# Optimization experiments

Hardware: AMD Instinct MI355X
Metric: run time of the kernel (lower is better)

Reference implementation:

```python
import jax, jax.numpy as jnp
import numpy as np

N, E, IN_DIM, HID, HEADS = 50000, 400000, 128, 64, 4
NEG_SLOPE, LN_EPS = 0.2, 1e-5


def setup_inputs() -> dict:
    key = jax.random.key(0)
    ks = jax.random.split(key, 12)
    x = jax.random.normal(ks[0], (N, IN_DIM), dtype=jnp.float32)
    edge_index = jax.random.randint(ks[1], (2, E), 0, N, dtype=jnp.int64)
    s = 1.0 / np.sqrt(HID)
    return {
        "x": x,
        "edge_index": edge_index,
        "W_gcn": jax.random.normal(ks[2], (IN_DIM, HID), dtype=jnp.float32) / np.sqrt(IN_DIM),
        "b_gcn": jnp.zeros((HID,), dtype=jnp.float32),
        "W_gat": jax.random.normal(ks[3], (HID, HEADS * HID), dtype=jnp.float32) * s,
        "att_src": jax.random.normal(ks[4], (HEADS, HID), dtype=jnp.float32) * s,
        "att_dst": jax.random.normal(ks[5], (HEADS, HID), dtype=jnp.float32) * s,
        "b_gat": jnp.zeros((HID,), dtype=jnp.float32),
        "W_patch": jax.random.normal(ks[6], (HID, HID), dtype=jnp.float32) * s,
        "b_patch": jnp.zeros((HID,), dtype=jnp.float32),
        "gamma": jnp.ones((HID,), dtype=jnp.float32),
        "beta": jnp.zeros((HID,), dtype=jnp.float32),
    }


def _forward(x, edge_index, W_gcn, b_gcn, W_gat, att_src, att_dst, b_gat,
             W_patch, b_patch, gamma, beta):
    n = x.shape[0]
    loop = jnp.arange(n, dtype=edge_index.dtype)
    src = jnp.concatenate([edge_index[0], loop])  # self-loops appended (PyG default)
    dst = jnp.concatenate([edge_index[1], loop])

    # ---- GCNConv: symmetric degree normalization + scatter-add ----
    deg = jax.ops.segment_sum(jnp.ones_like(dst, dtype=jnp.float32), dst, num_segments=n)
    dinv = jnp.where(deg > 0, jax.lax.rsqrt(deg), 0.0)
    norm = dinv[src] * dinv[dst]  # [E+N]
    xw = x @ W_gcn  # [N,HID]
    h1 = jax.ops.segment_sum(xw[src] * norm[:, None], dst, num_segments=n) + b_gcn
    h1 = jax.nn.relu(h1)

    # ---- GATConv (heads=4, concat=False -> mean over heads) ----
    z = (h1 @ W_gat).reshape(n, HEADS, HID)  # [N,H,C]
    a_s = jnp.einsum('nhc,hc->nh', z, att_src)  # [N,H]
    a_d = jnp.einsum('nhc,hc->nh', z, att_dst)
    e = jax.nn.leaky_relu(a_s[src] + a_d[dst], negative_slope=NEG_SLOPE)  # [E+N,H]
    # segment-softmax over incoming edges per destination node
    m = jax.ops.segment_max(e, dst, num_segments=n)  # [N,H]
    ex = jnp.exp(e - m[dst])
    denom = jax.ops.segment_sum(ex, dst, num_segments=n)
    alpha = ex / denom[dst]  # [E+N,H]
    agg = jax.ops.segment_sum(z[src] * alpha[:, :, None], dst, num_segments=n)  # [N,H,C]
    h2 = jax.nn.relu(agg.mean(axis=1) + b_gat)

    # ---- residual fusion + LayerNorm (dropout is identity in eval) ----
    h_patch = h1 @ W_patch + b_patch
    h = h1 + h2 + h_patch
    mu = h.mean(axis=-1, keepdims=True)
    var = h.var(axis=-1, keepdims=True)
    return (h - mu) * jax.lax.rsqrt(var + LN_EPS) * gamma + beta


def reference(x, edge_index, W_gcn, b_gcn, W_gat, att_src, att_dst, b_gat,
              W_patch, b_patch, gamma, beta):
    return _forward(x, edge_index, W_gcn, b_gcn, W_gat, att_src, att_dst, b_gat,
                    W_patch, b_patch, gamma, beta)
```

## Files before the change

### kernel.cpp

```cpp
#include <hip/hip_runtime.h>
#include <math.h>

#define IN_DIM 128
#define HID 64
#define HEADS 4
#define NEG_SLOPE 0.2f
#define LN_EPS 1e-5f
#define APAD 328

typedef short bf16x8 __attribute__((ext_vector_type(8)));
typedef float f32x4  __attribute__((ext_vector_type(4)));
typedef unsigned short u16x4 __attribute__((ext_vector_type(4)));
typedef unsigned long long ull;

__device__ inline unsigned short f2bf(float f) {
    unsigned u = __float_as_uint(f);
    u += 0x7fffu + ((u >> 16) & 1u);
    return (unsigned short)(u >> 16);
}
__device__ inline float bf2f(unsigned short s) {
    return __uint_as_float(((unsigned)s) << 16);
}
__device__ inline float leaky(float v) { return v > 0.0f ? v : NEG_SLOPE * v; }

__global__ __launch_bounds__(256) void k_init(const void* ei, int E, int n,
                           int* flag, int* hist, ull* A,
                           const float* __restrict__ Wg, const float* __restrict__ Wp,
                           const float* __restrict__ Wgcn,
                           const float* __restrict__ att_s, const float* __restrict__ att_d,
                           unsigned short* __restrict__ Wt_post,
                           unsigned short* __restrict__ Wt_xw,
                           float* __restrict__ w_s, float* __restrict__ w_d) {
    int t = threadIdx.x;
    int role = blockIdx.x;
    if (role < 14) {
        int p = role * 256 + t;
        if (p < 2560) {
            int c = p & 63, kg = p >> 6;
            bf16x8 v;
#pragma unroll
            for (int j = 0; j < 8; j++) {
                int k = kg * 8 + j;
                float f;
                if (k < 256) f = 0.25f * Wg[(size_t)(k & 63) * 256 + (k >> 6) * 64 + c];
                else         f = Wp[(size_t)(k - 256) * 64 + c];
                v[j] = (short)f2bf(f);
            }
            *(bf16x8*)(&Wt_post[(size_t)p * 8]) = v;
        } else if (p < 2560 + 1024) {
            int q = p - 2560;
            int c = q & 63, kg = q >> 6;
            bf16x8 v;
#pragma unroll
            for (int j = 0; j < 8; j++)
                v[j] = (short)f2bf(Wgcn[(size_t)(kg * 8 + j) * 64 + c]);
            *(bf16x8*)(&Wt_xw[(size_t)q * 8]) = v;
        }
        return;
    }
    if (role == 14) {
        A[t] = 0ULL;
        __shared__ int s_bad;
        if (t == 0) s_bad = 0;
        __syncthreads();
        int lim = E < 4096 ? E : 4096;
        int bad = 0;
        for (int k = t; k < lim; k += 256)
            if (((const ull*)ei)[k] >= (ull)n) bad = 1;
        if (bad) s_bad = 1;
        __syncthreads();
        if (t == 0) *flag = s_bad ? 0 : 1;
        int h = t >> 6, k = t & 63;
        float ss = 0.0f, sd = 0.0f;
        for (int c = 0; c < HID; c++) {
            float w = Wg[(size_t)k * (HEADS * HID) + h * HID + c];
            ss += w * att_s[h * HID + c];
            sd += w * att_d[h * HID + c];
        }
        w_s[h * HID + k] = ss;
        w_d[h * HID + k] = sd;
        return;
    }
    __shared__ int s_bad2;
    if (t == 0) s_bad2 = 0;
    __syncthreads();
    int lim = E < 4096 ? E : 4096;
    int bad = 0;
    for (int k = t; k < lim; k += 256)
        if (((const ull*)ei)[k] >= (ull)n) bad = 1;
    if (bad) s_bad2 = 1;
    __syncthreads();
    int is64 = s_bad2 ? 0 : 1;
    int hb = role - 15;
    int nhb = gridDim.x - 15;
    for (int i = hb * 256 + t; i < E; i += nhb * 256) {
        int d;
        if (is64) d = (int)((const long long*)ei)[E + i];
        else      d = ((const int*)ei)[E + i];
        atomicAdd(&hist[d], 1);
    }
}

__global__ __launch_bounds__(256) void k_scan_lb(const int* __restrict__ hist,
                                                 ull* __restrict__ A,
                                                 int* __restrict__ row_ptr,
                                                 int* __restrict__ cursor,
                                                 float* __restrict__ dinv, int n) {
    __shared__ int s[256];
    __shared__ int sbase;
    int t = threadIdx.x, c = blockIdx.x;
    int w = t >> 6, lane = t & 63;
    int i = c * 256 + t;
    int v = (i < n) ? hist[i] : 0;
    s[t] = v;
    __syncthreads();
    for (int off = 1; off < 256; off <<= 1) {
        int xv = (t >= off) ? s[t - off] : 0;
        __syncthreads();
        s[t] += xv;
        __syncthreads();
    }
    int incl = s[t];
    int S = s[255];
    if (t == 0) {
        if (c == 0) { sbase = 0; atomicExch(&A[0], (2ULL << 32) | (unsigned)S); }
        else          atomicExch(&A[c], (1ULL << 32) | (unsigned)S);
    }
    if (c > 0 && w == 0) {
        long long run = 0;
        int p = c - 1;
        for (;;) {
            int idx = p - lane;
            unsigned st, val;
            if (idx >= 0) {
                ull v2 = atomicAdd(&A[idx], 0ULL);
                st = (unsigned)(v2 >> 32); val = (unsigned)v2;
            } else { st = 2u; val = 0u; }
            ull pm = __ballot(st == 2);
            ull zm = __ballot(st == 0);
            int firstP = pm ? (__ffsll((long long)pm) - 1) : 64;
            int firstZ = zm ? (__ffsll((long long)zm) - 1) : 64;
            if (firstZ < firstP) { __builtin_amdgcn_s_sleep(1); continue; }
            unsigned contrib = (lane <= firstP) ? val : 0u;
#pragma unroll
            for (int o = 1; o <= 32; o <<= 1) contrib += __shfl_xor(contrib, o, 64);
            run += contrib;
            if (firstP < 64) break;
            p -= 64;
        }
        if (lane == 0) {
            sbase = (int)run;
            atomicExch(&A[c], (2ULL << 32) | (unsigned)(run + (unsigned)S));
        }
    }
    __syncthreads();
    if (i < n) {
        int excl = sbase + incl - v;
        row_ptr[i] = excl;
        cursor[i] = excl;
        dinv[i] = rsqrtf((float)(v + 1));
    }
}

__global__ __launch_bounds__(256) void k_scatter_xw(const void* ei, int E,
                                                    const int* __restrict__ flag,
                                                    int* __restrict__ cursor,
                                                    int* __restrict__ col,
                                                    const float* __restrict__ x,
                                                    const unsigned short* __restrict__ Wt_g,
                                                    const float* __restrict__ dinv,
                                                    unsigned short* __restrict__ xws, int n) {
    __shared__ unsigned short Wt[16 * 64 * 8];
    int nsb = (E + 255) >> 8;
    if ((int)blockIdx.x < nsb) {
        int i = blockIdx.x * 256 + threadIdx.x;
        if (i >= E) return;
        int is64 = *flag;
        int s, d;
        if (is64) { s = (int)((const long long*)ei)[i]; d = (int)((const long long*)ei)[E + i]; }
        else      { s = ((const int*)ei)[i];            d = ((const int*)ei)[E + i]; }
        int pos = atomicAdd(&cursor[d], 1);
        col[pos] = s;
    } else {
        int bx = blockIdx.x - nsb;
        int t = threadIdx.x;
        for (int idx = t; idx < 1024; idx += 256)
            *(bf16x8*)(&Wt[idx * 8]) = *(const bf16x8*)(&Wt_g[(size_t)idx * 8]);
        __syncthreads();
        int lane = t & 63;
        int li = lane & 15, quad = lane >> 4;
        int w = t >> 6;
        int r0 = bx * 64 + w * 16;
        int rload = r0 + li; if (rload > n - 1) rload = n - 1;
        f32x4 acc[4];
#pragma unroll
        for (int i = 0; i < 4; i++) acc[i] = (f32x4){0.f, 0.f, 0.f, 0.f};
        const float* xp = x + (size_t)rload * IN_DIM + quad * 8;
#pragma unroll
        for (int ks = 0; ks < 4; ks++) {
            float4 p0 = *(const float4*)(xp + ks * 32);
            float4 p1 = *(const float4*)(xp + ks * 32 + 4);
            bf16x8 a;
            a[0] = (short)f2bf(p0.x); a[1] = (short)f2bf(p0.y);
            a[2] = (short)f2bf(p0.z); a[3] = (short)f2bf(p0.w);
            a[4] = (short)f2bf(p1.x); a[5] = (short)f2bf(p1.y);
            a[6] = (short)f2bf(p1.z); a[7] = (short)f2bf(p1.w);
            int kg = ks * 4 + quad;
#pragma unroll
            for (int tt = 0; tt < 4; tt++) {
                bf16x8 bfr = *(const bf16x8*)(&Wt[((kg * 64) + tt * 16 + li) * 8]);
                acc[tt] = __builtin_amdgcn_mfma_f32_16x16x32_bf16(a, bfr, acc[tt], 0, 0, 0);
            }
        }
#pragma unroll
        for (int reg = 0; reg < 4; reg++) {
            int r = r0 + quad * 4 + reg;
            if (r >= n) continue;
            float dv = dinv[r];
#pragma unroll
            for (int tt = 0; tt < 4; tt++)
                xws[(size_t)r * HID + tt * 16 + li] = f2bf(acc[tt][reg] * dv);
        }
    }
}

__global__ __launch_bounds__(256) void k_gcn(const int* __restrict__ col,
                                             const int* __restrict__ row_ptr,
                                             const int* __restrict__ hist,
                                             const float* __restrict__ dinv,
                                             const unsigned short* __restrict__ xws,
                                             const float* __restrict__ b,
                                             const float* __restrict__ w_s,
                                             const float* __restrict__ w_d,
                                             unsigned short* __restrict__ h1b,
                                             float4* __restrict__ a_s,
                                             float4* __restrict__ a_d, int n) {
    int t = threadIdx.x;
    int w = t >> 6, lane = t & 63, q = lane >> 4, li = lane & 15;
    int d = blockIdx.x * 4 + w;
    if (d >= n) return;
    int start = row_ptr[d], cnt = hist[d];
    float a0, a1, a2, a3;
    {
        u16x4 sv = *(const u16x4*)(xws + (size_t)d * HID + li * 4);
        float z = (q == 0) ? 1.0f : 0.0f;
        a0 = z * bf2f(sv[0]); a1 = z * bf2f(sv[1]);
        a2 = z * bf2f(sv[2]); a3 = z * bf2f(sv[3]);
    }
    for (int base = 0; base < cnt; base += 64) {
        int m = cnt - base; if (m > 64) m = 64;
        int ci = (lane < m) ? col[start + base + lane] : 0;
        for (int kb = 0; kb < m; kb += 8) {
            int k0 = kb + q, k1 = kb + q + 4;
            int s0 = __shfl(ci, k0, 64);
            int s1 = __shfl(ci, k1 & 63, 64);
            u16x4 v0 = *(const u16x4*)(xws + (size_t)s0 * HID + li * 4);
            u16x4 v1 = *(const u16x4*)(xws + (size_t)s1 * HID + li * 4);
            float g0 = (k0 < m) ? 1.0f : 0.0f;
            float g1 = (k1 < m) ? 1.0f : 0.0f;
            a0 += g0 * bf2f(v0[0]) + g1 * bf2f(v1[0]);
            a1 += g0 * bf2f(v0[1]) + g1 * bf2f(v1[1]);
            a2 += g0 * bf2f(v0[2]) + g1 * bf2f(v1[2]);
            a3 += g0 * bf2f(v0[3]) + g1 * bf2f(v1[3]);
        }
    }
    a0 += __shfl_xor(a0, 16, 64); a1 += __shfl_xor(a1, 16, 64);
    a2 += __shfl_xor(a2, 16, 64); a3 += __shfl_xor(a3, 16, 64);
    a0 += __shfl_xor(a0, 32, 64); a1 += __shfl_xor(a1, 32, 64);
    a2 += __shfl_xor(a2, 32, 64); a3 += __shfl_xor(a3, 32, 64);
    float dv = dinv[d];
    float4 bv = *(const float4*)(b + li * 4);
    float h0 = fmaxf(a0 * dv + bv.x, 0.0f);
    float h1 = fmaxf(a1 * dv + bv.y, 0.0f);
    float h2 = fmaxf(a2 * dv + bv.z, 0.0f);
    float h3 = fmaxf(a3 * dv + bv.w, 0.0f);
    if (q == 0) {
        u16x4 o;
        o[0] = f2bf(h0); o[1] = f2bf(h1); o[2] = f2bf(h2); o[3] = f2bf(h3);
        *(u16x4*)(h1b + (size_t)d * HID + li * 4) = o;
    }
    float4 u  = *(const float4*)(w_s + q * 64 + li * 4);
    float vs = h0 * u.x + h1 * u.y + h2 * u.z + h3 * u.w;
    float4 u2 = *(const float4*)(w_d + q * 64 + li * 4);
    float vd = h0 * u2.x + h1 * u2.y + h2 * u2.z + h3 * u2.w;
#pragma unroll
    for (int o = 1; o <= 8; o <<= 1) {
        vs += __shfl_xor(vs, o, 64);
        vd += __shfl_xor(vd, o, 64);
    }
    float vs1 = __shfl(vs, 16, 64), vs2 = __shfl(vs, 32, 64), vs3 = __shfl(vs, 48, 64);
    float vd1 = __shfl(vd, 16, 64), vd2 = __shfl(vd, 32, 64), vd3 = __shfl(vd, 48, 64);
    if (lane == 0) {
        a_s[d] = make_float4(vs, vs1, vs2, vs3);
        a_d[d] = make_float4(vd, vd1, vd2, vd3);
    }
}

__global__ __launch_bounds__(256) void k_attn_post(
        const int* __restrict__ col, const int* __restrict__ row_ptr,
        const int* __restrict__ hist,
        const float4* __restrict__ a_s, const float4* __restrict__ a_d,
        const unsigned short* __restrict__ h1b,
        const unsigned short* __restrict__ Wt_g,
        const float* __restrict__ bp, const float* __restrict__ bg,
        const float* __restrict__ gamma, const float* __restrict__ beta,
        float* __restrict__ out, int n) {
    __shared__ unsigned short Atile[16 * APAD];
    __shared__ float hbuf[16 * 68];
    int t = threadIdx.x;
    int w = t >> 6, lane = t & 63, q = lane >> 4, li = lane & 15;
    int rowbase = blockIdx.x * 16;

    for (int j = 0; j < 4; j++) {
        int r = w * 4 + j;
        int d = rowbase + r;
        if (d >= n) {
            for (int c = lane; c < 320; c += 64) Atile[r * APAD + c] = 0;
            continue;
        }
        int start = row_ptr[d], cnt = hist[d];
        float4 ad = a_d[d];
        float4 asd = a_s[d];
        u16x4 sv = *(const u16x4*)(h1b + (size_t)d * HID + li * 4);
        float e0 = __expf(leaky(asd.x + ad.x));
        float e1 = __expf(leaky(asd.y + ad.y));
        float e2 = __expf(leaky(asd.z + ad.z));
        float e3 = __expf(leaky(asd.w + ad.w));
        float z = (q == 0) ? 1.0f : 0.0f;
        float f0 = bf2f(sv[0]), f1 = bf2f(sv[1]), f2 = bf2f(sv[2]), f3 = bf2f(sv[3]);
        f32x4 A0 = {z * e0 * f0, z * e0 * f1, z * e0 * f2, z * e0 * f3};
        f32x4 A1 = {z * e1 * f0, z * e1 * f1, z * e1 * f2, z * e1 * f3};
        f32x4 A2 = {z * e2 * f0, z * e2 * f1, z * e2 * f2, z * e2 * f3};
        f32x4 A3 = {z * e3 * f0, z * e3 * f1, z * e3 * f2, z * e3 * f3};
        float l0 = z * e0, l1 = z * e1, l2 = z * e2, l3 = z * e3;
        for (int base = 0; base < cnt; base += 64) {
            int m = cnt - base; if (m > 64) m = 64;
            int ci = (lane < m) ? col[start + base + lane] : 0;
            for (int kb = 0; kb < m; kb += 8) {
                int k0 = kb + q, k1 = kb + q + 4;
                int s0 = __shfl(ci, k0, 64);
                int s1 = __shfl(ci, k1 & 63, 64);
                float4 as0 = a_s[s0];
                float4 as1 = a_s[s1];
                u16x4 hv0 = *(const u16x4*)(h1b + (size_t)s0 * HID + li * 4);
                u16x4 hv1 = *(const u16x4*)(h1b + (size_t)s1 * HID + li * 4);
                bool p0 = (k0 < m), p1 = (k1 < m);
                float w00 = p0 ? __expf(leaky(as0.x + ad.x)) : 0.0f;
                float w01 = p0 ? __expf(leaky(as0.y + ad.y)) : 0.0f;
                float w02 = p0 ? __expf(leaky(as0.z + ad.z)) : 0.0f;
                float w03 = p0 ? __expf(leaky(as0.w + ad.w)) : 0.0f;
                float w10 = p1 ? __expf(leaky(as1.x + ad.x)) : 0.0f;
                float w11 = p1 ? __expf(leaky(as1.y + ad.y)) : 0.0f;
                float w12 = p1 ? __expf(leaky(as1.z + ad.z)) : 0.0f;
                float w13 = p1 ? __expf(leaky(as1.w + ad.w)) : 0.0f;
                float g00 = bf2f(hv0[0]), g01 = bf2f(hv0[1]);
                float g02 = bf2f(hv0[2]), g03 = bf2f(hv0[3]);
                float g10 = bf2f(hv1[0]), g11 = bf2f(hv1[1]);
                float g12 = bf2f(hv1[2]), g13 = bf2f(hv1[3]);
                A0[0] += w00 * g00 + w10 * g10; A0[1] += w00 * g01 + w10 * g11;
                A0[2] += w00 * g02 + w10 * g12; A0[3] += w00 * g03 + w10 * g13;
                A1[0] += w01 * g00 + w11 * g10; A1[1] += w01 * g01 + w11 * g11;
                A1[2] += w01 * g02 + w11 * g12; A1[3] += w01 * g03 + w11 * g13;
                A2[0] += w02 * g00 + w12 * g10; A2[1] += w02 * g01 + w12 * g11;
                A2[2] += w02 * g02 + w12 * g12; A2[3] += w02 * g03 + w12 * g13;
                A3[0] += w03 * g00 + w13 * g10; A3[1] += w03 * g01 + w13 * g11;
                A3[2] += w03 * g02 + w13 * g12; A3[3] += w03 * g03 + w13 * g13;
                l0 += w00 + w10; l1 += w01 + w11;
                l2 += w02 + w12; l3 += w03 + w13;
            }
        }
#pragma unroll
        for (int c4 = 0; c4 < 4; c4++) {
            A0[c4] += __shfl_xor(A0[c4], 16, 64);
            A1[c4] += __shfl_xor(A1[c4], 16, 64);
            A2[c4] += __shfl_xor(A2[c4], 16, 64);
            A3[c4] += __shfl_xor(A3[c4], 16, 64);
        }
        l0 += __shfl_xor(l0, 16, 64); l1 += __shfl_xor(l1, 16, 64);
        l2 += __shfl_xor(l2, 16, 64); l3 += __shfl_xor(l3, 16, 64);
#pragma unroll
        for (int c4 = 0; c4 < 4; c4++) {
            A0[c4] += __shfl_xor(A0[c4], 32, 64);
            A1[c4] += __shfl_xor(A1[c4], 32, 64);
            A2[c4] += __shfl_xor(A2[c4], 32, 64);
            A3[c4] += __shfl_xor(A3[c4], 32, 64);
        }
        l0 += __shfl_xor(l0, 32, 64); l1 += __shfl_xor(l1, 32, 64);
        l2 += __shfl_xor(l2, 32, 64); l3 += __shfl_xor(l3, 32, 64);
        f32x4 Aq; float lq;
        if (q == 0)      { Aq = A0; lq = l0; }
        else if (q == 1) { Aq = A1; lq = l1; }
        else if (q == 2) { Aq = A2; lq = l2; }
        else             { Aq = A3; lq = l3; }
        float inv = 1.0f / lq;
        u16x4 o;
        o[0] = f2bf(Aq[0] * inv); o[1] = f2bf(Aq[1] * inv);
        o[2] = f2bf(Aq[2] * inv); o[3] = f2bf(Aq[3] * inv);
        *(u16x4*)(&Atile[r * APAD + q * 64 + li * 4]) = o;
        if (q == 0) *(u16x4*)(&Atile[r * APAD + 256 + li * 4]) = sv;
    }
    __syncthreads();

    f32x4 acc_a = {0.f, 0.f, 0.f, 0.f}, acc_h = {0.f, 0.f, 0.f, 0.f};
#pragma unroll
    for (int ks = 0; ks < 10; ks++) {
        int kg = ks * 4 + q;
        bf16x8 a = *(const bf16x8*)(&Atile[li * APAD + ks * 32 + q * 8]);
        bf16x8 bb = *(const bf16x8*)(&Wt_g[(size_t)(kg * 64 + w * 16 + li) * 8]);
        if (ks < 8) acc_a = __builtin_amdgcn_mfma_f32_16x16x32_bf16(a, bb, acc_a, 0, 0, 0);
        else        acc_h = __builtin_amdgcn_mfma_f32_16x16x32_bf16(a, bb, acc_h, 0, 0, 0);
    }
    int cc = w * 16 + li;
    float bgv = bg[cc], bpv = bp[cc];
#pragma unroll
    for (int reg = 0; reg < 4; reg++) {
        int r = q * 4 + reg;
        float h1c = bf2f(Atile[r * APAD + 256 + cc]);
        float h2v = fmaxf(acc_a[reg] + bgv, 0.0f);
        hbuf[r * 68 + cc] = h1c + h2v + acc_h[reg] + bpv;
    }
    __syncthreads();

    int row = t >> 4, lj = t & 15;
    f32x4 hv4 = *(const f32x4*)(&hbuf[row * 68 + lj * 4]);
    float s1 = (hv4[0] + hv4[1]) + (hv4[2] + hv4[3]);
    float s2 = (hv4[0] * hv4[0] + hv4[1] * hv4[1]) + (hv4[2] * hv4[2] + hv4[3] * hv4[3]);
#pragma unroll
    for (int o = 1; o <= 8; o <<= 1) {
        s1 += __shfl_xor(s1, o, 64);
        s2 += __shfl_xor(s2, o, 64);
    }
    float mu = s1 * (1.0f / 64.0f);
    float var = s2 * (1.0f / 64.0f) - mu * mu;
    float rs = rsqrtf(var + LN_EPS);
    int rg = rowbase + row;
    if (rg < n) {
        float4 g4 = *(const float4*)(gamma + lj * 4);
        float4 b4 = *(const float4*)(beta + lj * 4);
        float4 ov;
        ov.x = (hv4[0] - mu) * rs * g4.x + b4.x;
        ov.y = (hv4[1] - mu) * rs * g4.y + b4.y;
        ov.z = (hv4[2] - mu) * rs * g4.z + b4.z;
        ov.w = (hv4[3] - mu) * rs * g4.w + b4.w;
        *(float4*)(out + (size_t)rg * HID + lj * 4) = ov;
    }
}

extern "C" void kernel_launch(void* const* d_in, const int* in_sizes, int n_in,
                              void* d_out, int out_size, void* d_ws, size_t ws_size,
                              hipStream_t stream) {
    int n = in_sizes[0] / IN_DIM;
    int E = in_sizes[1] / 2;

    const float* x     = (const float*)d_in[0];
    const void*  ei    = d_in[1];
    const float* W_gcn = (const float*)d_in[2];
    const float* b_gcn = (const float*)d_in[3];
    const float* W_gat = (const float*)d_in[4];
    const float* att_s = (const float*)d_in[5];
    const float* att_d = (const float*)d_in[6];
    const float* b_gat = (const float*)d_in[7];
    const float* W_p   = (const float*)d_in[8];
    const float* b_p   = (const float*)d_in[9];
    const float* gamma = (const float*)d_in[10];
    const float* beta  = (const float*)d_in[11];

    int n128 = ((n + 127) / 128) * 128;
    int nch  = (n + 255) / 256;
    int nsb  = (E + 255) / 256;
    int nhb  = nsb < 1024 ? nsb : 1024;
    if (nhb < 1) nhb = 1;

    float* ws = (float*)d_ws;
    size_t off = 0;
    int*   flag    = (int*)(ws + off);  off += 4;
    int*   hist    = (int*)(ws + off);  off += n;
    int*   row_ptr = (int*)(ws + off);  off += n;
    int*   cursor  = (int*)(ws + off);  off += n;
    int*   colv    = (int*)(ws + off);  off += E;
    float* dinv    = ws + off;          off += n;
    float* w_s     = ws + off;          off += HEADS * HID;
    float* w_d     = ws + off;          off += HEADS * HID;
    off = (off + 1) & ~(size_t)1;
    ull*   A       = (ull*)(ws + off);  off += 512;
    off = (off + 3) & ~(size_t)3;
    unsigned short* Wt_post = (unsigned short*)(ws + off); off += 2560 * 8 / 2;
    unsigned short* Wt_xw   = (unsigned short*)(ws + off); off += 1024 * 8 / 2;
    unsigned short* xws = (unsigned short*)(ws + off); off += (size_t)n * HID / 2;
    off = (off + 3) & ~(size_t)3;
    unsigned short* h1b = (unsigned short*)(ws + off); off += (size_t)n128 * HID / 2;
    off = (off + 3) & ~(size_t)3;
    float4* a_sv   = (float4*)(ws + off); off += (size_t)n * 4;
    float4* a_dv   = (float4*)(ws + off); off += (size_t)n * 4;

    hipMemsetAsync(hist, 0, (size_t)n * sizeof(int), stream);
    k_init<<<15 + nhb, 256, 0, stream>>>(ei, E, n, flag, hist, A,
                                         W_gat, W_p, W_gcn, att_s, att_d,
                                         Wt_post, Wt_xw, w_s, w_d);

    k_scan_lb<<<nch, 256, 0, stream>>>(hist, A, row_ptr, cursor, dinv, n);

    k_scatter_xw<<<nsb + (n + 63) / 64, 256, 0, stream>>>(ei, E, flag, cursor,
                                                          colv, x, Wt_xw,
                                                          dinv, xws, n);

    k_gcn<<<(n + 3) / 4, 256, 0, stream>>>(colv, row_ptr, hist, dinv, xws, b_gcn,
                                           w_s, w_d, h1b, a_sv, a_dv, n);

    k_attn_post<<<(n + 15) / 16, 256, 0, stream>>>(colv, row_ptr, hist, a_sv, a_dv,
                                                   h1b, Wt_post, b_p, b_gat,
                                                   gamma, beta, (float*)d_out, n);
}
```

Before: 219.9 us.

## Precompute per-edge attention exponentials in shared memory and unroll GCN gather

In the attention kernel, each block first computes exp(leaky(a_s[src]+a_d[dst])) once per edge for its 16 destination rows and stores the results in a shared-memory buffer. Before, all 16 lanes of each quarter-wave recomputed these four exponentials and reloaded a_s. The aggregation loop now reads the weights from shared memory, with a fallback to the old path when a block has more than 512 edges. The GCN aggregation loop is also unrolled to four gathered rows per step to raise memory-level parallelism. The cost is an extra barrier, a serial prefix scan by thread 0, and more registers.

After: 225.6 us. +2.6%, slower.

```diff
diff --git a/kernel.cpp b/kernel.cpp
--- a/kernel.cpp
+++ b/kernel.cpp
@@ -7,6 +7,7 @@
 #define NEG_SLOPE 0.2f
 #define LN_EPS 1e-5f
 #define APAD 328
+#define ECAP 512
 
 typedef short bf16x8 __attribute__((ext_vector_type(8)));
 typedef float f32x4  __attribute__((ext_vector_type(4)));
@@ -250,18 +251,24 @@
     for (int base = 0; base < cnt; base += 64) {
         int m = cnt - base; if (m > 64) m = 64;
         int ci = (lane < m) ? col[start + base + lane] : 0;
-        for (int kb = 0; kb < m; kb += 8) {
-            int k0 = kb + q, k1 = kb + q + 4;
-            int s0 = __shfl(ci, k0, 64);
+        for (int kb = 0; kb < m; kb += 16) {
+            int k0 = kb + q, k1 = kb + q + 4, k2 = kb + q + 8, k3 = kb + q + 12;
+            int s0 = __shfl(ci, k0 & 63, 64);
             int s1 = __shfl(ci, k1 & 63, 64);
+            int s2 = __shfl(ci, k2 & 63, 64);
+            int s3 = __shfl(ci, k3 & 63, 64);
             u16x4 v0 = *(const u16x4*)(xws + (size_t)s0 * HID + li * 4);
             u16x4 v1 = *(const u16x4*)(xws + (size_t)s1 * HID + li * 4);
+            u16x4 v2 = *(const u16x4*)(xws + (size_t)s2 * HID + li * 4);
+            u16x4 v3 = *(const u16x4*)(xws + (size_t)s3 * HID + li * 4);
             float g0 = (k0 < m) ? 1.0f : 0.0f;
             float g1 = (k1 < m) ? 1.0f : 0.0f;
-            a0 += g0 * bf2f(v0[0]) + g1 * bf2f(v1[0]);
-            a1 += g0 * bf2f(v0[1]) + g1 * bf2f(v1[1]);
-            a2 += g0 * bf2f(v0[2]) + g1 * bf2f(v1[2]);
-            a3 += g0 * bf2f(v0[3]) + g1 * bf2f(v1[3]);
+            float g2 = (k2 < m) ? 1.0f : 0.0f;
+            float g3 = (k3 < m) ? 1.0f : 0.0f;
+            a0 += (g0 * bf2f(v0[0]) + g1 * bf2f(v1[0])) + (g2 * bf2f(v2[0]) + g3 * bf2f(v3[0]));
+            a1 += (g0 * bf2f(v0[1]) + g1 * bf2f(v1[1])) + (g2 * bf2f(v2[1]) + g3 * bf2f(v3[1]));
+            a2 += (g0 * bf2f(v0[2]) + g1 * bf2f(v1[2])) + (g2 * bf2f(v2[2]) + g3 * bf2f(v3[2]));
+            a3 += (g0 * bf2f(v0[3]) + g1 * bf2f(v1[3])) + (g2 * bf2f(v2[3]) + g3 * bf2f(v3[3]));
         }
     }
     a0 += __shfl_xor(a0, 16, 64); a1 += __shfl_xor(a1, 16, 64);
@@ -306,10 +313,48 @@
         const float* __restrict__ gamma, const float* __restrict__ beta,
         float* __restrict__ out, int n) {
     __shared__ unsigned short Atile[16 * APAD];
-    __shared__ float hbuf[16 * 68];
+    __shared__ __align__(16) float wbuf[ECAP * 4];
+    __shared__ int sb[17];
+    __shared__ float4 sad[16];
+    float4* wls = (float4*)wbuf;
+    float*  hbuf = wbuf;
     int t = threadIdx.x;
     int w = t >> 6, lane = t & 63, q = lane >> 4, li = lane & 15;
     int rowbase = blockIdx.x * 16;
+
+    if (t == 0) {
+        int bptr = row_ptr[rowbase < n ? rowbase : n - 1];
+        sb[0] = bptr;
+        for (int j = 0; j < 16; j++) {
+            int d = rowbase + j;
+            bptr += (d < n) ? hist[d] : 0;
+            sb[j + 1] = bptr;
+        }
+    }
+    if (t < 16) {
+        int d = rowbase + t;
+        sad[t] = (d < n) ? a_d[d] : make_float4(0.f, 0.f, 0.f, 0.f);
+    }
+    __syncthreads();
+    int start0 = sb[0];
+    int totc = sb[16] - start0;
+    bool fast = (totc <= ECAP);
+    if (fast) {
+        for (int e = t; e < totc; e += 256) {
+            int s = col[start0 + e];
+            int j = 0;
+#pragma unroll
+            for (int jj = 1; jj < 16; jj++) j += (e >= (sb[jj] - start0)) ? 1 : 0;
+            float4 as = a_s[s], ad = sad[j];
+            float4 wv;
+            wv.x = __expf(leaky(as.x + ad.x));
+            wv.y = __expf(leaky(as.y + ad.y));
+            wv.z = __expf(leaky(as.z + ad.z));
+            wv.w = __expf(leaky(as.w + ad.w));
+            wls[e] = wv;
+        }
+    }
+    __syncthreads();
 
     for (int j = 0; j < 4; j++) {
         int r = w * 4 + j;
@@ -319,7 +364,8 @@
             continue;
         }
         int start = row_ptr[d], cnt = hist[d];
-        float4 ad = a_d[d];
+        int rel = start - start0;
+        float4 ad = sad[r];
         float4 asd = a_s[d];
         u16x4 sv = *(const u16x4*)(h1b + (size_t)d * HID + li * 4);
         float e0 = __expf(leaky(asd.x + ad.x));
@@ -336,37 +382,69 @@
         for (int base = 0; base < cnt; base += 64) {
             int m = cnt - base; if (m > 64) m = 64;
             int ci = (lane < m) ? col[start + base + lane] : 0;
-            for (int kb = 0; kb < m; kb += 8) {
-                int k0 = kb + q, k1 = kb + q + 4;
-                int s0 = __shfl(ci, k0, 64);
-                int s1 = __shfl(ci, k1 & 63, 64);
-                float4 as0 = a_s[s0];
-                float4 as1 = a_s[s1];
-                u16x4 hv0 = *(const u16x4*)(h1b + (size_t)s0 * HID + li * 4);
-                u16x4 hv1 = *(const u16x4*)(h1b + (size_t)s1 * HID + li * 4);
-                bool p0 = (k0 < m), p1 = (k1 < m);
-                float w00 = p0 ? __expf(leaky(as0.x + ad.x)) : 0.0f;
-                float w01 = p0 ? __expf(leaky(as0.y + ad.y)) : 0.0f;
-                float w02 = p0 ? __expf(leaky(as0.z + ad.z)) : 0.0f;
-                float w03 = p0 ? __expf(leaky(as0.w + ad.w)) : 0.0f;
-                float w10 = p1 ? __expf(leaky(as1.x + ad.x)) : 0.0f;
-                float w11 = p1 ? __expf(leaky(as1.y + ad.y)) : 0.0f;
-                float w12 = p1 ? __expf(leaky(as1.z + ad.z)) : 0.0f;
-                float w13 = p1 ? __expf(leaky(as1.w + ad.w)) : 0.0f;
-                float g00 = bf2f(hv0[0]), g01 = bf2f(hv0[1]);
-                float g02 = bf2f(hv0[2]), g03 = bf2f(hv0[3]);
-                float g10 = bf2f(hv1[0]), g11 = bf2f(hv1[1]);
-                float g12 = bf2f(hv1[2]), g13 = bf2f(hv1[3]);
-                A0[0] += w00 * g00 + w10 * g10; A0[1] += w00 * g01 + w10 * g11;
-                A0[2] += w00 * g02 + w10 * g12; A0[3] += w00 * g03 + w10 * g13;
-                A1[0] += w01 * g00 + w11 * g10; A1[1] += w01 * g01 + w11 * g11;
-                A1[2] += w01 * g02 + w11 * g12; A1[3] += w01 * g03 + w11 * g13;
-                A2[0] += w02 * g00 + w12 * g10; A2[1] += w02 * g01 + w12 * g11;
-                A2[2] += w02 * g02 + w12 * g12; A2[3] += w02 * g03 + w12 * g13;
-                A3[0] += w03 * g00 + w13 * g10; A3[1] += w03 * g01 + w13 * g11;
-                A3[2] += w03 * g02 + w13 * g12; A3[3] += w03 * g03 + w13 * g13;
-                l0 += w00 + w10; l1 += w01 + w11;
-                l2 += w02 + w12; l3 += w03 + w13;
+            if (fast) {
+                for (int kb = 0; kb < m; kb += 8) {
+                    int k0 = kb + q, k1 = kb + q + 4;
+                    int s0 = __shfl(ci, k0 & 63, 64);
+                    int s1 = __shfl(ci, k1 & 63, 64);
+                    bool p0 = (k0 < m), p1 = (k1 < m);
+                    float4 wl0 = wls[p0 ? (rel + base + k0) : 0];
+                    float4 wl1 = wls[p1 ? (rel + base + k1) : 0];
+                    u16x4 hv0 = *(const u16x4*)(h1b + (size_t)s0 * HID + li * 4);
+                    u16x4 hv1 = *(const u16x4*)(h1b + (size_t)s1 * HID + li * 4);
+                    float g0 = p0 ? 1.0f : 0.0f, g1 = p1 ? 1.0f : 0.0f;
+                    float w00 = wl0.x * g0, w01 = wl0.y * g0;
+                    float w02 = wl0.z * g0, w03 = wl0.w * g0;
+                    float w10 = wl1.x * g1, w11 = wl1.y * g1;
+                    float w12 = wl1.z * g1, w13 = wl1.w * g1;
+                    float g00 = bf2f(hv0[0]), g01 = bf2f(hv0[1]);
+                    float g02 = bf2f(hv0[2]), g03 = bf2f(hv0[3]);
+                    float g10 = bf2f(hv1[0]), g11 = bf2f(hv1[1]);
+                    float g12 = bf2f(hv1[2]), g13 = bf2f(hv1[3]);
+                    A0[0] += w00 * g00 + w10 * g10; A0[1] += w00 * g01 + w10 * g11;
+                    A0[2] += w00 * g02 + w10 * g12; A0[3] += w00 * g03 + w10 * g13;
+                    A1[0] += w01 * g00 + w11 * g10; A1[1] += w01 * g01 + w11 * g11;
+                    A1[2] += w01 * g02 + w11 * g12; A1[3] += w01 * g03 + w11 * g13;
+                    A2[0] += w02 * g00 + w12 * g10; A2[1] += w02 * g01 + w12 * g11;
+                    A2[2] += w02 * g02 + w12 * g12; A2[3] += w02 * g03 + w12 * g13;
+                    A3[0] += w03 * g00 + w13 * g10; A3[1] += w03 * g01 + w13 * g11;
+                    A3[2] += w03 * g02 + w13 * g12; A3[3] += w03 * g03 + w13 * g13;
+                    l0 += w00 + w10; l1 += w01 + w11;
+                    l2 += w02 + w12; l3 += w03 + w13;
+                }
+            } else {
+                for (int kb = 0; kb < m; kb += 8) {
+                    int k0 = kb + q, k1 = kb + q + 4;
+                    int s0 = __shfl(ci, k0 & 63, 64);
+                    int s1 = __shfl(ci, k1 & 63, 64);
+                    float4 as0 = a_s[s0];
+                    float4 as1 = a_s[s1];
+                    u16x4 hv0 = *(const u16x4*)(h1b + (size_t)s0 * HID + li * 4);
+                    u16x4 hv1 = *(const u16x4*)(h1b + (size_t)s1 * HID + li * 4);
+                    bool p0 = (k0 < m), p1 = (k1 < m);
+                    float w00 = p0 ? __expf(leaky(as0.x + ad.x)) : 0.0f;
+                    float w01 = p0 ? __expf(leaky(as0.y + ad.y)) : 0.0f;
+                    float w02 = p0 ? __expf(leaky(as0.z + ad.z)) : 0.0f;
+                    float w03 = p0 ? __expf(leaky(as0.w + ad.w)) : 0.0f;
+                    float w10 = p1 ? __expf(leaky(as1.x + ad.x)) : 0.0f;
+                    float w11 = p1 ? __expf(leaky(as1.y + ad.y)) : 0.0f;
+                    float w12 = p1 ? __expf(leaky(as1.z + ad.z)) : 0.0f;
+                    float w13 = p1 ? __expf(leaky(as1.w + ad.w)) : 0.0f;
+                    float g00 = bf2f(hv0[0]), g01 = bf2f(hv0[1]);
+                    float g02 = bf2f(hv0[2]), g03 = bf2f(hv0[3]);
+                    float g10 = bf2f(hv1[0]), g11 = bf2f(hv1[1]);
+                    float g12 = bf2f(hv1[2]), g13 = bf2f(hv1[3]);
+                    A0[0] += w00 * g00 + w10 * g10; A0[1] += w00 * g01 + w10 * g11;
+                    A0[2] += w00 * g02 + w10 * g12; A0[3] += w00 * g03 + w10 * g13;
+                    A1[0] += w01 * g00 + w11 * g10; A1[1] += w01 * g01 + w11 * g11;
+                    A1[2] += w01 * g02 + w11 * g12; A1[3] += w01 * g03 + w11 * g13;
+                    A2[0] += w02 * g00 + w12 * g10; A2[1] += w02 * g01 + w12 * g11;
+                    A2[2] += w02 * g02 + w12 * g12; A2[3] += w02 * g03 + w12 * g13;
+                    A3[0] += w03 * g00 + w13 * g10; A3[1] += w03 * g01 + w13 * g11;
+                    A3[2] += w03 * g02 + w13 * g12; A3[3] += w03 * g03 + w13 * g13;
+                    l0 += w00 + w10; l1 += w01 + w11;
+                    l2 += w02 + w12; l3 += w03 + w13;
+                }
             }
         }
 #pragma unroll
```
